# Kernel optimization log

Hardware: AMD Instinct MI355X
Metric: run time of the kernel (lower is better)

The kernel has to match this reference:

```python
import jax, jax.numpy as jnp
import numpy as np

HEAD_DIM = 64
N_HEADS = 25
N_KV_HEADS = 5
WINDOW = 1024
N_META = 128
EPS = 1e-6
ROPE_BASE = 10000.0


def _rmsnorm(x, w):
    # per-head RMSNorm over last dim, computed in fp32 (matches HymbaRMSNorm)
    xf = x.astype(jnp.float32)
    var = jnp.mean(xf * xf, axis=-1, keepdims=True)
    return w * (xf * jax.lax.rsqrt(var + EPS)).astype(x.dtype)


def _rotate_half(x):
    x1, x2 = jnp.split(x, 2, axis=-1)
    return jnp.concatenate((-x2, x1), axis=-1)


def _rope_cos_sin(position_ids):
    # equivalent to indexing the cached cos/sin tables with position_ids
    inv_freq = 1.0 / (ROPE_BASE ** (jnp.arange(0, HEAD_DIM, 2, dtype=jnp.float32) / HEAD_DIM))
    freqs = position_ids.astype(jnp.float32)[..., None] * inv_freq  # [B,T,hd/2]
    emb = jnp.concatenate((freqs, freqs), axis=-1)                   # [B,T,hd]
    return jnp.cos(emb)[:, None], jnp.sin(emb)[:, None]              # [B,1,T,hd]


def setup_inputs() -> dict:
    key = jax.random.key(0)
    k1, k2, k3, k4, k5 = jax.random.split(key, 5)
    B, T = 2, 2048
    return {
        "query_states": jax.random.normal(k1, (B, T, N_HEADS * HEAD_DIM), dtype=jnp.float32),
        "key_states": jax.random.normal(k2, (B, T, N_KV_HEADS * HEAD_DIM), dtype=jnp.float32),
        "value_states": jax.random.normal(k3, (B, T, N_KV_HEADS * HEAD_DIM), dtype=jnp.float32),
        "q_norm_w": jax.random.uniform(k4, (HEAD_DIM,), dtype=jnp.float32, minval=0.5, maxval=1.5),
        "k_norm_w": jax.random.uniform(k5, (HEAD_DIM,), dtype=jnp.float32, minval=0.5, maxval=1.5),
        "position_ids": jnp.broadcast_to(jnp.arange(T, dtype=jnp.int32), (B, T)),
    }


def reference(query_states, key_states, value_states, q_norm_w, k_norm_w, position_ids):
    B, T, _ = query_states.shape
    # [B, H, T, hd]
    q = query_states.reshape(B, T, N_HEADS, HEAD_DIM).transpose(0, 2, 1, 3)
    k = key_states.reshape(B, T, N_KV_HEADS, HEAD_DIM).transpose(0, 2, 1, 3)
    v = value_states.reshape(B, T, N_KV_HEADS, HEAD_DIM).transpose(0, 2, 1, 3)

    # per-head QK RMSNorm
    q = _rmsnorm(q, q_norm_w)
    k = _rmsnorm(k, k_norm_w)

    # RoPE
    cos, sin = _rope_cos_sin(position_ids)
    q = q * cos + _rotate_half(q) * sin
    k = k * cos + _rotate_half(k) * sin

    # GQA: repeat each kv head num_heads // num_kv_heads times (consecutively)
    n_rep = N_HEADS // N_KV_HEADS
    k_e = jnp.repeat(k, n_rep, axis=1)
    v_e = jnp.repeat(v, n_rep, axis=1)

    scale = 1.0 / np.sqrt(HEAD_DIM)
    scores = jnp.einsum("bhqd,bhkd->bhqk", q, k_e) * scale

    # SWA mask: causal AND (in sliding window OR meta/memory token)
    q_idx = jnp.arange(T)[:, None]
    k_idx = jnp.arange(T)[None, :]
    attend = (k_idx <= q_idx) & ((k_idx >= q_idx - WINDOW + 1) | (k_idx < N_META))
    scores = jnp.where(attend, scores, -jnp.inf)

    attn_weights = jax.nn.softmax(scores, axis=-1)
    out = jnp.einsum("bhqk,bhkd->bhqd", attn_weights, v_e)
    return out.transpose(0, 2, 1, 3).reshape(B, T, N_HEADS * HEAD_DIM)
```

## Files before the change

### kernel.cpp

```cpp
#include <hip/hip_runtime.h>
#include <cmath>

typedef float  f32x4  __attribute__((ext_vector_type(4)));
typedef __bf16 bf16x8 __attribute__((ext_vector_type(8)));
typedef unsigned int u32x4 __attribute__((ext_vector_type(4)));
typedef unsigned int u32x2 __attribute__((ext_vector_type(2)));
typedef unsigned int   u32;
typedef unsigned short u16;

#define HEAD_DIM 64
#define N_HEADS  25
#define N_KV     5
#define WINDOW   1024
#define N_META   128
#define B_       2
#define T_       2048
#define QB       64
#define NTILES   (T_ / 64)
#define TILE_U32 2048
#define SM_BIAS  (-20.0f)

static __device__ __forceinline__ u16 bf16_bits(float f) {
  __bf16 h = (__bf16)f;
  return __builtin_bit_cast(u16, h);
}
static __device__ __forceinline__ u32 pack2(float lo, float hi) {
  return ((u32)bf16_bits(hi) << 16) | bf16_bits(lo);
}
static __device__ __forceinline__ float fexp2(float x) {
  return __builtin_amdgcn_exp2f(x);
}
static __device__ __forceinline__ void gload16(const u32* g, u32* l) {
  __builtin_amdgcn_global_load_lds((const __attribute__((address_space(1))) u32*)g,
                                   (__attribute__((address_space(3))) u32*)l, 16, 0, 0);
}

__global__ __launch_bounds__(256) void prep_kernel(
    const float* __restrict__ k_in, const float* __restrict__ k_w,
    const float* __restrict__ v_in, const int* __restrict__ pos_ids,
    u32* __restrict__ k_ws, u32* __restrict__ v_ws)
{
  const int blk = blockIdx.x;
  const int tid = threadIdx.x;

  if (blk < B_ * N_KV * NTILES) {
    int tile = blk & (NTILES - 1);
    int bk   = blk >> 5;
    int kvh  = bk % N_KV, b = bk / N_KV;
    int t0   = tile * 64;

    __shared__ u16 Tl[64][72];

    #pragma unroll
    for (int it = 0; it < 4; ++it) {
      int idx = it * 256 + tid;
      int kl = idx >> 4, dq = idx & 15;
      const float4 f = *(const float4*)&v_in[((size_t)(b * T_ + t0 + kl)) * (N_KV * HEAD_DIM) + kvh * HEAD_DIM + dq * 4];
      Tl[dq * 4 + 0][kl] = bf16_bits(f.x);
      Tl[dq * 4 + 1][kl] = bf16_bits(f.y);
      Tl[dq * 4 + 2][kl] = bf16_bits(f.z);
      Tl[dq * 4 + 3][kl] = bf16_bits(f.w);
    }
    __syncthreads();

    u32* outb = v_ws + (size_t)blk * TILE_U32;
    #pragma unroll
    for (int it = 0; it < 8; ++it) {
      int o = it * 256 + tid;
      int d = o >> 5, c = o & 31;
      u32 w = ((u32)Tl[d][2 * c + 1] << 16) | Tl[d][2 * c];
      int a = c >> 4, bs = (c >> 3) & 1, gp = (c >> 1) & 3, e = c & 1;
      int sp = (4 * a + gp) ^ (d & 7);
      outb[d * 32 + sp * 4 + 2 * bs + e] = w;
    }
    return;
  }

  int gw   = (((blk - B_ * N_KV * NTILES) * 256 + tid) >> 6);
  int lane = tid & 63;
  if (gw >= B_ * T_ * N_KV) return;
  int kvh = gw % N_KV;
  int bt  = gw / N_KV;

  float x = k_in[(size_t)bt * (N_KV * HEAD_DIM) + kvh * HEAD_DIM + lane];
  float ss = x * x;
  #pragma unroll
  for (int off = 32; off; off >>= 1) ss += __shfl_xor(ss, off);
  float y = k_w[lane] * x * rsqrtf(ss * (1.f / 64.f) + 1e-6f);

  int   pos = pos_ids[bt];
  float ang = (float)pos * powf(10000.f, -(float)(lane & 31) * (1.f / 32.f));
  float c, s;
  sincosf(ang, &s, &c);
  float part = __shfl_xor(y, 32);
  float r = (lane < 32) ? (y * c - part * s) : (y * c + part * s);

  u16 mybits = bf16_bits(r);
  u32 pb = (u32)(u16)__shfl_xor((int)mybits, 1);
  u32 w  = (pb << 16) | mybits;
  int b = bt / T_, t = bt % T_;
  if (!(lane & 1)) {
    int c32 = lane >> 1;
    int kl = t & 63, tile = t >> 6;
    int sp = (c32 >> 2) ^ (kl & 7);
    k_ws[(((size_t)(b * N_KV + kvh) * NTILES + tile)) * TILE_U32 + kl * 32 + sp * 4 + (c32 & 3)] = w;
  }
}

__global__ __launch_bounds__(256, 4) void attn_kernel(
    const float* __restrict__ q_in, const float* __restrict__ q_w,
    const int* __restrict__ pos_ids,
    const u32* __restrict__ kws, const u32* __restrict__ vws,
    float* __restrict__ out)
{
  const int i  = blockIdx.x;
  const int x  = i & 7, k = i >> 3;
  const int gA = (5 * x) >> 2;
  const int a0 = 200 * x - 160 * gA;
  const int nB = 40 + a0;
  int grp, j_;
  if (k < nB) { grp = gA + 1; j_ = k; }
  else        { grp = gA;     j_ = a0 + (k - nB); }
  const int qt  = 31 - j_ / 5;
  const int hh  = j_ % 5;
  const int b   = grp / 5;
  const int kvh = grp % 5;
  const int h   = kvh * 5 + hh;
  const int qb  = qt * QB;
  const int tid = threadIdx.x, wid = tid >> 6, lane = tid & 63;
  const int l15 = lane & 15, g = lane >> 4;
  const int qrow0 = wid * 16;

  __shared__ u32 Ks[TILE_U32];
  __shared__ u32 Vt[TILE_U32];

  const int nt    = (qt <= 18) ? (qt + 1) : 19;
  const int shift = qt - 18;

  const size_t kvbase = ((size_t)(b * N_KV + kvh)) * NTILES * TILE_U32;
  const u32* kb = kws + kvbase;
  const u32* vb = vws + kvbase;

  #pragma unroll
  for (int j = 0; j < 2; ++j) {
    int ci = (wid << 1) | j;
    gload16(kb + ci * 256 + lane * 4, &Ks[ci * 256]);
  }

  {
    const int   jbase = (4 * l15) & 31;
    const float r32   = 0.74989420933f;
    float fr[4];
    fr[0] = powf(10000.f, -(float)jbase * (1.f / 32.f));
    fr[1] = fr[0] * r32; fr[2] = fr[1] * r32; fr[3] = fr[2] * r32;

    const int t0g = b * T_ + qb + qrow0;
    int pos_prev = pos_ids[t0g + g];
    float cc[4], sn[4], c4[4], s4[4];
    #pragma unroll
    for (int e = 0; e < 4; ++e) {
      sincosf((float)pos_prev * fr[e], &sn[e], &cc[e]);
      sincosf(4.f * fr[e], &s4[e], &c4[e]);
    }
    const float4 wv = *(const float4*)&q_w[4 * l15];
    #pragma unroll
    for (int it = 0; it < 4; ++it) {
      const int row = 4 * it + g;
      if (it) {
        int pos = pos_ids[t0g + row];
        if (__all(pos == pos_prev + 4)) {
          #pragma unroll
          for (int e = 0; e < 4; ++e) {
            float c2 = cc[e] * c4[e] - sn[e] * s4[e];
            sn[e] = sn[e] * c4[e] + cc[e] * s4[e];
            cc[e] = c2;
          }
        } else {
          #pragma unroll
          for (int e = 0; e < 4; ++e) sincosf((float)pos * fr[e], &sn[e], &cc[e]);
        }
        pos_prev = pos;
      }
      const float4 xv = *(const float4*)&q_in[((size_t)(t0g + row)) * (N_HEADS * HEAD_DIM) + h * HEAD_DIM + 4 * l15];
      float ss = xv.x * xv.x + xv.y * xv.y + xv.z * xv.z + xv.w * xv.w;
      ss += __shfl_xor(ss, 1); ss += __shfl_xor(ss, 2);
      ss += __shfl_xor(ss, 4); ss += __shfl_xor(ss, 8);
      const float rn = rsqrtf(ss * (1.f / 64.f) + 1e-6f);
      float y[4] = {wv.x * xv.x * rn, wv.y * xv.y * rn, wv.z * xv.z * rn, wv.w * xv.w * rn};
      float rv[4];
      #pragma unroll
      for (int e = 0; e < 4; ++e) {
        float part = __shfl_xor(y[e], 8);
        rv[e] = ((l15 < 8) ? (y[e] * cc[e] - part * sn[e])
                           : (y[e] * cc[e] + part * sn[e])) * 0.18033688f;
      }
      u32x2 w2;
      w2.x = pack2(rv[0], rv[1]);
      w2.y = pack2(rv[2], rv[3]);
      *(u32x2*)&Vt[(qrow0 + row) * 32 + 2 * l15] = w2;
    }
  }
  __syncthreads();

  bf16x8 qf[2];
  #pragma unroll
  for (int ks = 0; ks < 2; ++ks)
    qf[ks] = *(const bf16x8*)&Vt[(qrow0 + l15) * 32 + 16 * ks + 4 * g];
  __syncthreads();

  #pragma unroll
  for (int j = 0; j < 2; ++j) {
    int ci = (wid << 1) | j;
    gload16(vb + ci * 256 + lane * 4, &Vt[ci * 256]);
  }

  f32x4 acc_o[4];
  #pragma unroll
  for (int mt = 0; mt < 4; ++mt) acc_o[mt] = (f32x4)(0.f);
  f32x4 acc_l = (f32x4)(0.f);

  u32x4 onesw;
  onesw.x = 0x3F803F80u; onesw.y = 0x3F803F80u; onesw.z = 0x3F803F80u; onesw.w = 0x3F803F80u;
  const bf16x8 vones = __builtin_bit_cast(bf16x8, onesw);

  const int q_abs = qb + qrow0 + l15;

  for (int i2 = 0; i2 < nt; ++i2) {
    const int k0 = ((qt <= 18 || i2 < 2) ? i2 : i2 + shift) << 6;
    int tn = -1;
    if (i2 + 1 < nt) tn = (qt <= 18 || i2 + 1 < 2) ? (i2 + 1) : (i2 + 1 + shift);

    f32x4 accs[4];
    #pragma unroll
    for (int mt = 0; mt < 4; ++mt) accs[mt] = (f32x4)(SM_BIAS);
    #pragma unroll
    for (int ks = 0; ks < 2; ++ks) {
      #pragma unroll
      for (int mt = 0; mt < 4; ++mt) {
        bf16x8 kf = *(const bf16x8*)&Ks[(16 * mt + l15) * 32 + (((4 * ks + g) ^ (l15 & 7)) << 2)];
        accs[mt] = __builtin_amdgcn_mfma_f32_16x16x32_bf16(kf, qf[ks], accs[mt], 0, 0, 0);
      }
    }

    const bool do_mask = (i2 == nt - 1) || (qt >= 18 && i2 == 2);
    if (do_mask) {
      #pragma unroll
      for (int mt = 0; mt < 4; ++mt)
        #pragma unroll
        for (int rg = 0; rg < 4; ++rg) {
          int key = k0 + 16 * mt + 4 * g + rg;
          bool ok = (key <= q_abs) && ((key >= q_abs - (WINDOW - 1)) || (key < N_META));
          accs[mt][rg] = ok ? accs[mt][rg] : -INFINITY;
        }
    }
    #pragma unroll
    for (int mt = 0; mt < 4; ++mt)
      #pragma unroll
      for (int rg = 0; rg < 4; ++rg)
        accs[mt][rg] = fexp2(accs[mt][rg]);

    __syncthreads();

    if (tn >= 0) {
      const u32* kt = kb + (size_t)tn * TILE_U32;
      #pragma unroll
      for (int j = 0; j < 2; ++j) {
        int ci = (wid << 1) | j;
        gload16(kt + ci * 256 + lane * 4, &Ks[ci * 256]);
      }
    }

    #pragma unroll
    for (int ks2 = 0; ks2 < 2; ++ks2) {
      const int m0 = 2 * ks2, m1 = 2 * ks2 + 1;
      u32x4 aw;
      aw.x = pack2(accs[m0][0], accs[m0][1]);
      aw.y = pack2(accs[m0][2], accs[m0][3]);
      aw.z = pack2(accs[m1][0], accs[m1][1]);
      aw.w = pack2(accs[m1][2], accs[m1][3]);
      bf16x8 af = __builtin_bit_cast(bf16x8, aw);
      acc_l = __builtin_amdgcn_mfma_f32_16x16x32_bf16(af, vones, acc_l, 0, 0, 0);
      #pragma unroll
      for (int mt2 = 0; mt2 < 4; ++mt2) {
        bf16x8 vf = *(const bf16x8*)&Vt[(16 * mt2 + l15) * 32 + (((4 * ks2 + g) ^ (l15 & 7)) << 2)];
        acc_o[mt2] = __builtin_amdgcn_mfma_f32_16x16x32_bf16(af, vf, acc_o[mt2], 0, 0, 0);
      }
    }

    __syncthreads();

    if (tn >= 0) {
      const u32* vt = vb + (size_t)tn * TILE_U32;
      #pragma unroll
      for (int j = 0; j < 2; ++j) {
        int ci = (wid << 1) | j;
        gload16(vt + ci * 256 + lane * 4, &Vt[ci * 256]);
      }
    }
  }

  #pragma unroll
  for (int mt2 = 0; mt2 < 4; ++mt2)
    #pragma unroll
    for (int rg = 0; rg < 4; ++rg) {
      int t = qb + qrow0 + 4 * g + rg;
      out[((size_t)(b * T_ + t)) * (N_HEADS * HEAD_DIM) + h * HEAD_DIM + 16 * mt2 + l15] =
          acc_o[mt2][rg] / acc_l[rg];
    }
}

extern "C" void kernel_launch(void* const* d_in, const int* in_sizes, int n_in,
                              void* d_out, int out_size, void* d_ws, size_t ws_size,
                              hipStream_t stream) {
  const float* q   = (const float*)d_in[0];
  const float* k   = (const float*)d_in[1];
  const float* v   = (const float*)d_in[2];
  const float* qw  = (const float*)d_in[3];
  const float* kw  = (const float*)d_in[4];
  const int*   pos = (const int*)d_in[5];

  u32* kp = (u32*)d_ws;
  u32* vp = kp + (size_t)B_ * N_KV * NTILES * TILE_U32;
  float* outp = (float*)d_out;

  prep_kernel<<<B_ * N_KV * NTILES + 5120, 256, 0, stream>>>(k, kw, v, pos, kp, vp);
  attn_kernel<<<1600, 256, 0, stream>>>(q, qw, pos, kp, vp, outp);
}
```

Baseline: 55.40 us.

## Restructure K-prep to use float4 rows and incremental RoPE rotation

The K-normalization and RoPE path of the prep kernel now has each wave process 16 consecutive tokens, four rows at a time, with each lane handling four contiguous head dims through float4 loads. Sines and cosines are seeded once per lane and then advanced by a fixed angle-addition rotation whenever positions step by four, falling back to a direct sincos otherwise. Outputs are written as packed 64-bit stores, and the grid shrinks from 5120 K blocks to 320. This cuts per-element transcendental work and launch size, at the cost of small rounding drift from the recurrence at large angles.

```diff
diff --git a/kernel.cpp b/kernel.cpp
--- a/kernel.cpp
+++ b/kernel.cpp
@@ -76,34 +76,71 @@
     return;
   }
 
-  int gw   = (((blk - B_ * N_KV * NTILES) * 256 + tid) >> 6);
-  int lane = tid & 63;
-  if (gw >= B_ * T_ * N_KV) return;
-  int kvh = gw % N_KV;
-  int bt  = gw / N_KV;
-
-  float x = k_in[(size_t)bt * (N_KV * HEAD_DIM) + kvh * HEAD_DIM + lane];
-  float ss = x * x;
-  #pragma unroll
-  for (int off = 32; off; off >>= 1) ss += __shfl_xor(ss, off);
-  float y = k_w[lane] * x * rsqrtf(ss * (1.f / 64.f) + 1e-6f);
-
-  int   pos = pos_ids[bt];
-  float ang = (float)pos * powf(10000.f, -(float)(lane & 31) * (1.f / 32.f));
-  float c, s;
-  sincosf(ang, &s, &c);
-  float part = __shfl_xor(y, 32);
-  float r = (lane < 32) ? (y * c - part * s) : (y * c + part * s);
-
-  u16 mybits = bf16_bits(r);
-  u32 pb = (u32)(u16)__shfl_xor((int)mybits, 1);
-  u32 w  = (pb << 16) | mybits;
-  int b = bt / T_, t = bt % T_;
-  if (!(lane & 1)) {
-    int c32 = lane >> 1;
-    int kl = t & 63, tile = t >> 6;
-    int sp = (c32 >> 2) ^ (kl & 7);
-    k_ws[(((size_t)(b * N_KV + kvh) * NTILES + tile)) * TILE_U32 + kl * 32 + sp * 4 + (c32 & 3)] = w;
+  const int lane = tid & 63, wid = tid >> 6;
+  const int l15 = lane & 15, g = lane >> 4;
+  const int gw   = (blk - B_ * N_KV * NTILES) * 4 + wid;
+  const int bkvh = gw >> 7;
+  const int sl   = gw & 127;
+  const int b    = bkvh / N_KV, kvh = bkvh % N_KV;
+  const int t0   = sl * 16;
+
+  const int   jbase = (4 * l15) & 31;
+  const float r32   = 0.74989420933f;
+  float fr[4];
+  fr[0] = powf(10000.f, -(float)jbase * (1.f / 32.f));
+  fr[1] = fr[0] * r32; fr[2] = fr[1] * r32; fr[3] = fr[2] * r32;
+
+  const int t0g = b * T_ + t0;
+  int pos_prev = pos_ids[t0g + g];
+  float cc[4], sn[4], c4[4], s4[4];
+  #pragma unroll
+  for (int e = 0; e < 4; ++e) {
+    sincosf((float)pos_prev * fr[e], &sn[e], &cc[e]);
+    sincosf(4.f * fr[e], &s4[e], &c4[e]);
+  }
+  const float4 wv = *(const float4*)&k_w[4 * l15];
+  u32* outb = k_ws + ((size_t)bkvh * NTILES + (t0 >> 6)) * TILE_U32;
+  const int klbase = t0 & 63;
+  const int sp_c   = l15 >> 1;
+  const int slot   = (2 * l15) & 3;
+
+  #pragma unroll
+  for (int it = 0; it < 4; ++it) {
+    const int row = 4 * it + g;
+    if (it) {
+      int pos = pos_ids[t0g + row];
+      if (__all(pos == pos_prev + 4)) {
+        #pragma unroll
+        for (int e = 0; e < 4; ++e) {
+          float c2 = cc[e] * c4[e] - sn[e] * s4[e];
+          sn[e] = sn[e] * c4[e] + cc[e] * s4[e];
+          cc[e] = c2;
+        }
+      } else {
+        #pragma unroll
+        for (int e = 0; e < 4; ++e) sincosf((float)pos * fr[e], &sn[e], &cc[e]);
+      }
+      pos_prev = pos;
+    }
+    const float4 xv = *(const float4*)&k_in[((size_t)(t0g + row)) * (N_KV * HEAD_DIM) + kvh * HEAD_DIM + 4 * l15];
+    float ss = xv.x * xv.x + xv.y * xv.y + xv.z * xv.z + xv.w * xv.w;
+    ss += __shfl_xor(ss, 1); ss += __shfl_xor(ss, 2);
+    ss += __shfl_xor(ss, 4); ss += __shfl_xor(ss, 8);
+    const float rn = rsqrtf(ss * (1.f / 64.f) + 1e-6f);
+    float y[4] = {wv.x * xv.x * rn, wv.y * xv.y * rn, wv.z * xv.z * rn, wv.w * xv.w * rn};
+    float rv[4];
+    #pragma unroll
+    for (int e = 0; e < 4; ++e) {
+      float part = __shfl_xor(y[e], 8);
+      rv[e] = (l15 < 8) ? (y[e] * cc[e] - part * sn[e])
+                        : (y[e] * cc[e] + part * sn[e]);
+    }
+    const int kl = klbase + row;
+    const int sp = sp_c ^ (kl & 7);
+    u32x2 w2;
+    w2.x = pack2(rv[0], rv[1]);
+    w2.y = pack2(rv[2], rv[3]);
+    *(u32x2*)&outb[kl * 32 + sp * 4 + slot] = w2;
   }
 }
 
@@ -323,6 +360,6 @@
   u32* vp = kp + (size_t)B_ * N_KV * NTILES * TILE_U32;
   float* outp = (float*)d_out;
 
-  prep_kernel<<<B_ * N_KV * NTILES + 5120, 256, 0, stream>>>(k, kw, v, pos, kp, vp);
+  prep_kernel<<<2 * B_ * N_KV * NTILES, 256, 0, stream>>>(k, kw, v, pos, kp, vp);
   attn_kernel<<<1600, 256, 0, stream>>>(q, qw, pos, kp, vp, outp);
 }
```

Result: faster. 52.58 us (-5.1%).
